# Optimization experiments

Measured on AMD Instinct MI355X. Metric: run time of the kernel, lower is better.

The kernel has to match this reference:

```python
import jax, jax.numpy as jnp
import numpy as np
from jax import lax

FEATURE_NUM = 16
FILTERS = 64
BATCH = 64
WINDOW = 5
T = 2048
SECTORS = 11
D = 256          # embedding dim / number of quantization buckets
DA = 64
VOCAB = 100000
L = T - 3 * WINDOW + 3  # 2036, length after conv->maxpool->conv (all valid, stride 1)
BN_EPS = 1e-5


def _conv1d(x, w):
    # x: [N, C, W], w: [O, I, K], valid padding, stride 1
    return lax.conv_general_dilated(x, w, (1,), 'VALID', dimension_numbers=('NCH', 'OIH', 'NCH'))


def setup_inputs() -> dict:
    key = jax.random.key(0)
    ks = jax.random.split(key, 9)
    x = jax.random.normal(ks[0], (BATCH, 2 * FEATURE_NUM, T), jnp.float32)
    conv1_w = jax.random.normal(ks[1], (FILTERS, 2 * FEATURE_NUM, WINDOW), jnp.float32) * 0.1
    conv1_b = jnp.zeros((FILTERS,), jnp.float32)
    bn_gamma = jnp.ones((FILTERS,), jnp.float32)
    bn_beta = jnp.zeros((FILTERS,), jnp.float32)
    conv2_w = jax.random.normal(ks[2], (1, FILTERS, WINDOW), jnp.float32) * 0.1
    conv2_b = jnp.zeros((1,), jnp.float32)
    emb = jax.random.normal(ks[3], (VOCAB, D), jnp.float32)
    W1 = jax.random.normal(ks[4], (DA, L), jnp.float32)
    W2 = jax.random.normal(ks[5], (DA, 1), jnp.float32)
    lin_w = jax.random.normal(ks[6], (SECTORS, D), jnp.float32) * 0.05
    lin_b = jnp.zeros((SECTORS,), jnp.float32)
    return {'x': x, 'conv1_w': conv1_w, 'conv1_b': conv1_b, 'bn_gamma': bn_gamma,
            'bn_beta': bn_beta, 'conv2_w': conv2_w, 'conv2_b': conv2_b, 'emb': emb,
            'W1': W1, 'W2': W2, 'lin_w': lin_w, 'lin_b': lin_b}


def reference(x, conv1_w, conv1_b, bn_gamma, bn_beta, conv2_w, conv2_b, emb, W1, W2, lin_w, lin_b):
    # conv1 (valid) -> maxpool(k=WINDOW, s=1) -> batchnorm (train-mode batch stats) -> conv2 -> relu
    h = _conv1d(x, conv1_w) + conv1_b[None, :, None]                     # [B, F, T-W+1]
    h = lax.reduce_window(h, -jnp.inf, lax.max, (1, 1, WINDOW), (1, 1, 1), 'VALID')
    mu = jnp.mean(h, axis=(0, 2), keepdims=True)
    var = jnp.mean((h - mu) ** 2, axis=(0, 2), keepdims=True)            # biased, as torch BN train
    h = (h - mu) * lax.rsqrt(var + BN_EPS) * bn_gamma[None, :, None] + bn_beta[None, :, None]
    h = jax.nn.relu(_conv1d(h, conv2_w) + conv2_b[None, :, None])        # [B, 1, L]
    c = jax.nn.sigmoid(h[:, 0, :])                                       # [B, L] in (0,1)
    # embedding_generate: first j with c <= (j+1)/D  <=>  j = ceil(c*D) - 1
    idx = jnp.clip(jnp.ceil(c * D).astype(jnp.int32) - 1, 0, D - 1)      # [B, L]
    e = emb[idx]                                                         # [B, L, D]
    # per-sample attention: A = W2^T tanh(W1 @ out), batched as einsums
    t = jnp.tanh(jnp.einsum('al,bld->bad', W1, e))                       # [B, DA, D]
    A = jnp.einsum('a,bad->bd', W2[:, 0], t)                             # [B, D]
    att = jax.nn.softmax(jnp.einsum('bld,bd->bl', e, A), axis=1)         # [B, L]
    scores = A @ lin_w.T + lin_b                                         # [B, SECTORS]
    return att, scores
```

## Files before the change

kernel.cpp:

```cpp
#include <hip/hip_runtime.h>
#include <hip/hip_bf16.h>
#include <math.h>

#define BATCH 64
#define CIN   32
#define TIN   2048
#define FILT  64
#define WIN   5
#define TP1   2044
#define TP2   2040
#define LOUT  2036
#define DEMB  256
#define DA    64
#define NSEC  11
#define NC    4
#define CS    509
#define TILE_T 252

__global__ __launch_bounds__(256) void k_conv1pool(
    const float* __restrict__ x, const float* __restrict__ w1,
    const float* __restrict__ b1, float* __restrict__ h2,
    float* __restrict__ bnps, float* __restrict__ bnpq) {
  __shared__ float xl[CIN * 264];
  const int b   = blockIdx.y;
  const int t0  = blockIdx.x * TILE_T;
  const int tid = threadIdx.x;

  for (int i = tid; i < CIN * 264; i += 256) {
    int c = i / 264, o = i - c * 264;
    int gt = t0 + o;
    float v = 0.f;
    if (o < 260 && gt < TIN) v = x[(b * CIN + c) * TIN + gt];
    xl[i] = v;
  }
  __syncthreads();

  const int tg  = tid & 63;
  const int tb  = tg * 4;
  const int wf0 = __builtin_amdgcn_readfirstlane(tid >> 6) * 16;
  const float* wb = w1 + wf0 * (CIN * WIN);

  float acc[16][4];
#pragma unroll
  for (int ff = 0; ff < 16; ++ff) {
    float bias = b1[wf0 + ff];
    acc[ff][0] = bias; acc[ff][1] = bias; acc[ff][2] = bias; acc[ff][3] = bias;
  }

  for (int c = 0; c < CIN; ++c) {
    float4 xa  = *(const float4*)&xl[c * 264 + tb];
    float4 xb4 = *(const float4*)&xl[c * 264 + tb + 4];
    float xw[8] = {xa.x, xa.y, xa.z, xa.w, xb4.x, xb4.y, xb4.z, xb4.w};
#pragma unroll
    for (int ff = 0; ff < 16; ++ff) {
      const float* wr = wb + ff * (CIN * WIN) + c * WIN;
#pragma unroll
      for (int k = 0; k < WIN; ++k) {
        float wv = wr[k];
        acc[ff][0] = fmaf(xw[k + 0], wv, acc[ff][0]);
        acc[ff][1] = fmaf(xw[k + 1], wv, acc[ff][1]);
        acc[ff][2] = fmaf(xw[k + 2], wv, acc[ff][2]);
        acc[ff][3] = fmaf(xw[k + 3], wv, acc[ff][3]);
      }
    }
  }

  const bool rowvalid = (tg < 63);
  const int blk = blockIdx.y * 9 + blockIdx.x;
#pragma unroll
  for (int ff = 0; ff < 16; ++ff) {
    float n0 = __shfl_down(acc[ff][0], 1);
    float n1 = __shfl_down(acc[ff][1], 1);
    float n2 = __shfl_down(acc[ff][2], 1);
    float n3 = __shfl_down(acc[ff][3], 1);
    float h[8] = {acc[ff][0], acc[ff][1], acc[ff][2], acc[ff][3], n0, n1, n2, n3};
    float o0 = fmaxf(fmaxf(fmaxf(h[0], h[1]), fmaxf(h[2], h[3])), h[4]);
    float o1 = fmaxf(fmaxf(fmaxf(h[1], h[2]), fmaxf(h[3], h[4])), h[5]);
    float o2 = fmaxf(fmaxf(fmaxf(h[2], h[3]), fmaxf(h[4], h[5])), h[6]);
    float o3 = fmaxf(fmaxf(fmaxf(h[3], h[4]), fmaxf(h[5], h[6])), h[7]);
    const int f = wf0 + ff;
    float s = 0.f, q = 0.f;
    const int t2b = t0 + tb;
    if (rowvalid && (t2b + 3 < TP2)) {
      *(float4*)&h2[(b * FILT + f) * TP2 + t2b] = make_float4(o0, o1, o2, o3);
      s = o0 + o1 + o2 + o3;
      q = o0 * o0 + o1 * o1 + o2 * o2 + o3 * o3;
    } else if (rowvalid) {
      float ov[4] = {o0, o1, o2, o3};
#pragma unroll
      for (int j = 0; j < 4; ++j) {
        int t2 = t2b + j;
        if (t2 < TP2) { h2[(b * FILT + f) * TP2 + t2] = ov[j]; s += ov[j]; q += ov[j] * ov[j]; }
      }
    }
#pragma unroll
    for (int off = 32; off > 0; off >>= 1) {
      s += __shfl_down(s, off);
      q += __shfl_down(q, off);
    }
    if (tg == 0) { bnps[blk * FILT + f] = s; bnpq[blk * FILT + f] = q; }
  }
}

__global__ void k_bnfin(const float* __restrict__ bnps, const float* __restrict__ bnpq,
                        const float* __restrict__ gamma, const float* __restrict__ beta,
                        const float* __restrict__ w2, const float* __restrict__ b2,
                        double* __restrict__ ws2, double* __restrict__ c0p) {
  const int f = threadIdx.x;
  double s = 0.0, q = 0.0;
  for (int blk = 0; blk < 576; ++blk) {
    s += (double)bnps[blk * FILT + f];
    q += (double)bnpq[blk * FILT + f];
  }
  const double N = (double)(BATCH * TP2);
  double mu  = s / N;
  double var = q / N - mu * mu;
  double sc  = (double)gamma[f] / sqrt(var + 1e-5);
  double sh  = (double)beta[f] - mu * sc;
  double wsum = 0.0;
#pragma unroll
  for (int k = 0; k < WIN; ++k) {
    double wv = (double)w2[f * WIN + k];
    ws2[f * WIN + k] = sc * wv;
    wsum += wv;
  }
  double part = sh * wsum;
#pragma unroll
  for (int off = 32; off > 0; off >>= 1) part += __shfl_down(part, off);
  if (f == 0) c0p[0] = part + (double)b2[0];
}

__global__ __launch_bounds__(256) void k_conv2(
    const float* __restrict__ h2, const double* __restrict__ ws2,
    const double* __restrict__ c0p, int* __restrict__ idxp, int* __restrict__ count) {
  __shared__ float hl[FILT * 260];
  __shared__ int hist[DEMB];
  const int b = blockIdx.y;
  const int t0 = blockIdx.x * 256;
  const int tid = threadIdx.x;
  for (int i = tid; i < FILT * 260; i += 256) {
    int f = i / 260, o = i - f * 260;
    int gt = t0 + o;
    hl[i] = (gt < TP2) ? h2[(b * FILT + f) * TP2 + gt] : 0.f;
  }
  hist[tid] = 0;
  __syncthreads();
  const int t = t0 + tid;
  if (t < LOUT) {
    double z = c0p[0];
    for (int f = 0; f < FILT; ++f) {
      const double* wr = ws2 + f * WIN;
      z = fma((double)hl[f * 260 + tid + 0], wr[0], z);
      z = fma((double)hl[f * 260 + tid + 1], wr[1], z);
      z = fma((double)hl[f * 260 + tid + 2], wr[2], z);
      z = fma((double)hl[f * 260 + tid + 3], wr[3], z);
      z = fma((double)hl[f * 260 + tid + 4], wr[4], z);
    }
    z = z > 0.0 ? z : 0.0;
    double c = 1.0 / (1.0 + exp(-z));
    int iv = (int)ceil(c * 256.0) - 1;
    iv = min(max(iv, 0), DEMB - 1);
    idxp[b * LOUT + t] = iv;
    atomicAdd(&hist[iv], 1);
  }
  __syncthreads();
  atomicAdd(&count[b * DEMB + tid], hist[tid]);
}

__global__ void k_t1(const float* __restrict__ W1, float* __restrict__ W1T) {
  int i = blockIdx.x * 256 + threadIdx.x;
  int l = i >> 6, a = i & 63;
  W1T[i] = W1[a * LOUT + l];
}
__global__ void k_t2(const float* __restrict__ emb, float* __restrict__ embT) {
  int i = blockIdx.x * 256 + threadIdx.x;
  int d = i >> 8, j = i & 255;
  embT[i] = emb[j * DEMB + d];
}

__global__ __launch_bounds__(256) void k_sbuild(
    const int* __restrict__ idxp, const float* __restrict__ w1t,
    float* __restrict__ Sg) {
  __shared__ float S[DA * 257];
  __shared__ int il[512];
  const int b = blockIdx.y, ch = blockIdx.x;
  const int tid = threadIdx.x;
  for (int i = tid; i < DA * 257; i += 256) S[i] = 0.f;
  const int l0 = ch * CS;
  for (int i = tid; i < CS; i += 256) il[i] = idxp[b * LOUT + l0 + i];
  __syncthreads();
  const int a = tid & 63, w = tid >> 6;
#pragma unroll 4
  for (int li = w; li < CS; li += 4) {
    int j = il[li];
    float v = w1t[(l0 + li) * DA + a];
    atomicAdd(&S[a * 257 + j], v);
  }
  __syncthreads();
  for (int i = tid; i < DA * DEMB; i += 256) {
    int aa = i >> 8, j = i & 255;
    Sg[((b * NC + ch) * DA + aa) * DEMB + j] = S[aa * 257 + j];
  }
}

__global__ __launch_bounds__(256) void k_gemmA(
    const float* __restrict__ Sg, const float* __restrict__ emb,
    const float* __restrict__ W2, float* __restrict__ Avec) {
  __shared__ float Al[16 * 64];
  __shared__ float Bl[16 * 64];
  __shared__ float red[16 * 64];
  const int b = blockIdx.x, c0 = blockIdx.y * 64;
  const int tid = threadIdx.x;
  const int tx = tid & 15, ty = tid >> 4;
  const int sa = tid >> 2, skq = (tid & 3) * 4;
  const int bk = tid >> 4, bseg = tid & 15;
  float acc[4][4] = {{0}};

  for (int kc = 0; kc < 16; ++kc) {
    const int kb = kc * 16;
    float4 v0 = *(const float4*)&Sg[((b * NC + 0) * DA + sa) * DEMB + kb + skq];
    float4 v1 = *(const float4*)&Sg[((b * NC + 1) * DA + sa) * DEMB + kb + skq];
    float4 v2 = *(const float4*)&Sg[((b * NC + 2) * DA + sa) * DEMB + kb + skq];
    float4 v3 = *(const float4*)&Sg[((b * NC + 3) * DA + sa) * DEMB + kb + skq];
    float4 sv = make_float4(v0.x + v1.x + v2.x + v3.x, v0.y + v1.y + v2.y + v3.y,
                            v0.z + v1.z + v2.z + v3.z, v0.w + v1.w + v2.w + v3.w);
    Al[(skq + 0) * 64 + sa] = sv.x;
    Al[(skq + 1) * 64 + sa] = sv.y;
    Al[(skq + 2) * 64 + sa] = sv.z;
    Al[(skq + 3) * 64 + sa] = sv.w;
    float4 e4 = *(const float4*)&emb[(kb + bk) * DEMB + c0 + bseg * 4];
    *(float4*)&Bl[bk * 64 + bseg * 4] = e4;
    __syncthreads();
#pragma unroll
    for (int k = 0; k < 16; ++k) {
      float4 av = *(const float4*)&Al[k * 64 + ty * 4];
      float4 bv = *(const float4*)&Bl[k * 64 + tx * 4];
      acc[0][0] = fmaf(av.x, bv.x, acc[0][0]); acc[0][1] = fmaf(av.x, bv.y, acc[0][1]);
      acc[0][2] = fmaf(av.x, bv.z, acc[0][2]); acc[0][3] = fmaf(av.x, bv.w, acc[0][3]);
      acc[1][0] = fmaf(av.y, bv.x, acc[1][0]); acc[1][1] = fmaf(av.y, bv.y, acc[1][1]);
      acc[1][2] = fmaf(av.y, bv.z, acc[1][2]); acc[1][3] = fmaf(av.y, bv.w, acc[1][3]);
      acc[2][0] = fmaf(av.z, bv.x, acc[2][0]); acc[2][1] = fmaf(av.z, bv.y, acc[2][1]);
      acc[2][2] = fmaf(av.z, bv.z, acc[2][2]); acc[2][3] = fmaf(av.z, bv.w, acc[2][3]);
      acc[3][0] = fmaf(av.w, bv.x, acc[3][0]); acc[3][1] = fmaf(av.w, bv.y, acc[3][1]);
      acc[3][2] = fmaf(av.w, bv.z, acc[3][2]); acc[3][3] = fmaf(av.w, bv.w, acc[3][3]);
    }
    __syncthreads();
  }
  float cs[4] = {0.f, 0.f, 0.f, 0.f};
#pragma unroll
  for (int r = 0; r < 4; ++r) {
    float wv = W2[ty * 4 + r];
#pragma unroll
    for (int j = 0; j < 4; ++j) cs[j] += tanhf(acc[r][j]) * wv;
  }
#pragma unroll
  for (int j = 0; j < 4; ++j) red[ty * 64 + tx * 4 + j] = cs[j];
  __syncthreads();
  if (tid < 64) {
    float s = 0.f;
#pragma unroll
    for (int q = 0; q < 16; ++q) s += red[q * 64 + tid];
    Avec[b * DEMB + c0 + tid] = s;
  }
}

__global__ __launch_bounds__(256) void k_att(
    const float* __restrict__ Avec, const float* __restrict__ embT,
    const int* __restrict__ count, const float* __restrict__ linw,
    const float* __restrict__ linb, float* __restrict__ p,
    float* __restrict__ scores) {
  __shared__ float Al[DEMB];
  __shared__ float scratch[4];
  const int b = blockIdx.x, j = threadIdx.x;
  Al[j] = Avec[b * DEMB + j];
  __syncthreads();
  float dot = 0.f;
  for (int d = 0; d < DEMB; ++d) dot = fmaf(embT[d * DEMB + j], Al[d], dot);
  const int cnt = count[b * DEMB + j];
  float v = (cnt > 0) ? dot : -3.4e38f;
#pragma unroll
  for (int off = 32; off > 0; off >>= 1) v = fmaxf(v, __shfl_down(v, off));
  if ((j & 63) == 0) scratch[j >> 6] = v;
  __syncthreads();
  const float m = fmaxf(fmaxf(scratch[0], scratch[1]), fmaxf(scratch[2], scratch[3]));
  __syncthreads();
  float e = (cnt > 0) ? expf(dot - m) : 0.f;
  float zs = e * (float)cnt;
#pragma unroll
  for (int off = 32; off > 0; off >>= 1) zs += __shfl_down(zs, off);
  if ((j & 63) == 0) scratch[j >> 6] = zs;
  __syncthreads();
  const float Z = scratch[0] + scratch[1] + scratch[2] + scratch[3];
  p[b * DEMB + j] = (cnt > 0) ? e / Z : 0.f;
  for (int s = 0; s < NSEC; ++s) {
    __syncthreads();
    float part = Al[j] * linw[s * DEMB + j];
#pragma unroll
    for (int off = 32; off > 0; off >>= 1) part += __shfl_down(part, off);
    if ((j & 63) == 0) scratch[j >> 6] = part;
    __syncthreads();
    if (j == 0)
      scores[b * NSEC + s] = scratch[0] + scratch[1] + scratch[2] + scratch[3] + linb[s];
  }
}

__global__ void k_gather(const int* __restrict__ idxp, const float* __restrict__ p,
                         float* __restrict__ att) {
  const int b = blockIdx.y;
  const int t = blockIdx.x * 256 + threadIdx.x;
  if (t < LOUT) att[b * LOUT + t] = p[b * DEMB + idxp[b * LOUT + t]];
}

extern "C" void kernel_launch(void* const* d_in, const int* in_sizes, int n_in,
                              void* d_out, int out_size, void* d_ws, size_t ws_size,
                              hipStream_t stream) {
  const float* x      = (const float*)d_in[0];
  const float* w1     = (const float*)d_in[1];
  const float* b1     = (const float*)d_in[2];
  const float* gamma  = (const float*)d_in[3];
  const float* beta   = (const float*)d_in[4];
  const float* w2     = (const float*)d_in[5];
  const float* b2     = (const float*)d_in[6];
  const float* emb    = (const float*)d_in[7];
  const float* W1     = (const float*)d_in[8];
  const float* W2     = (const float*)d_in[9];
  const float* linw   = (const float*)d_in[10];
  const float* linb   = (const float*)d_in[11];

  char* ws = (char*)d_ws;
  int*    count = (int*)   (ws + 0);
  double* ws2   = (double*)(ws + 65536);
  double* c0p   = (double*)(ws + 68096);
  float*  bnps  = (float*) (ws + 68608);
  float*  bnpq  = (float*) (ws + 216064);
  int*    idxp  = (int*)   (ws + 363520);
  float*  w1t   = (float*) (ws + 884736);
  float*  embT  = (float*) (ws + 1405952);
  float*  Avec  = (float*) (ws + 1668096);
  float*  p     = (float*) (ws + 1733632);
  float*  h2    = (float*) (ws + 1799168);
  float*  Sg    = (float*) (ws + 35222528);

  float* att_out    = (float*)d_out;
  float* scores_out = (float*)d_out + BATCH * LOUT;

  hipMemsetAsync(count, 0, 65536, stream);
  k_t1<<<dim3(509), 256, 0, stream>>>(W1, w1t);
  k_t2<<<dim3(256), 256, 0, stream>>>(emb, embT);
  k_conv1pool<<<dim3(9, 64), 256, 0, stream>>>(x, w1, b1, h2, bnps, bnpq);
  k_bnfin<<<dim3(1), 64, 0, stream>>>(bnps, bnpq, gamma, beta, w2, b2, ws2, c0p);
  k_conv2<<<dim3(8, 64), 256, 0, stream>>>(h2, ws2, c0p, idxp, count);
  k_sbuild<<<dim3(NC, 64), 256, 0, stream>>>(idxp, w1t, Sg);
  k_gemmA<<<dim3(64, 4), 256, 0, stream>>>(Sg, emb, W2, Avec);
  k_att<<<dim3(64), 256, 0, stream>>>(Avec, embT, count, linw, linb, p, scores_out);
  k_gather<<<dim3(8, 64), 256, 0, stream>>>(idxp, p, att_out);
}
```

Baseline: 359.1 us.

## Merge prep kernels, split conv1 over filter halves, fuse gather into attention

Replaces the memset and two transpose kernels with one prep kernel that zeroes counts, transposes W1 and emb through LDS tiles, and reorders conv1 weights channel-major. Conv1 gets a third grid dimension splitting the filters into two halves, which doubles block count and halves accumulator registers. BN finalize now uses 256 threads to parallelize the partial-sum reduction, and the att gather is folded into k_att using LDS probabilities. Together these cut launch count and aim to improve occupancy and memory coalescing, at the cost of each conv1 block reloading the x tile twice.

```diff
diff --git a/kernel.cpp b/kernel.cpp
--- a/kernel.cpp
+++ b/kernel.cpp
@@ -17,8 +17,44 @@
 #define CS    509
 #define TILE_T 252
 
+__global__ __launch_bounds__(256) void k_prep(
+    const float* __restrict__ W1, const float* __restrict__ emb,
+    const float* __restrict__ w1, float* __restrict__ w1t,
+    float* __restrict__ embT, float* __restrict__ w1r, int* __restrict__ count) {
+  __shared__ float tl[64 * 65];
+  int bk = blockIdx.x;
+  const int tid = threadIdx.x;
+  if (bk < 64) { count[bk * 256 + tid] = 0; return; }
+  bk -= 64;
+  if (bk < 32) {
+    const int l0 = bk * 64;
+    const int lc = tid & 63, rq = tid >> 6;
+    for (int a = rq; a < 64; a += 4)
+      tl[a * 65 + lc] = (l0 + lc < LOUT) ? W1[a * LOUT + l0 + lc] : 0.f;
+    __syncthreads();
+    for (int lp = rq; lp < 64; lp += 4)
+      if (l0 + lp < LOUT) w1t[(l0 + lp) * 64 + lc] = tl[lc * 65 + lp];
+    return;
+  }
+  bk -= 32;
+  if (bk < 16) {
+    const int j0 = (bk & 3) * 64, d0 = (bk >> 2) * 64;
+    const int c = tid & 63, rq = tid >> 6;
+    for (int j = rq; j < 64; j += 4) tl[j * 65 + c] = emb[(j0 + j) * DEMB + d0 + c];
+    __syncthreads();
+    for (int d = rq; d < 64; d += 4) embT[(d0 + d) * DEMB + j0 + c] = tl[c * 65 + d];
+    return;
+  }
+  bk -= 16;
+  {
+    int i = bk * 256 + tid;
+    int c = i / 320, r = i - c * 320, f = r / 5, k = r - f * 5;
+    w1r[i] = w1[f * (CIN * WIN) + c * WIN + k];
+  }
+}
+
 __global__ __launch_bounds__(256) void k_conv1pool(
-    const float* __restrict__ x, const float* __restrict__ w1,
+    const float* __restrict__ x, const float* __restrict__ w1r,
     const float* __restrict__ b1, float* __restrict__ h2,
     float* __restrict__ bnps, float* __restrict__ bnpq) {
   __shared__ float xl[CIN * 264];
@@ -37,12 +73,11 @@
 
   const int tg  = tid & 63;
   const int tb  = tg * 4;
-  const int wf0 = __builtin_amdgcn_readfirstlane(tid >> 6) * 16;
-  const float* wb = w1 + wf0 * (CIN * WIN);
-
-  float acc[16][4];
-#pragma unroll
-  for (int ff = 0; ff < 16; ++ff) {
+  const int wf0 = __builtin_amdgcn_readfirstlane((int)blockIdx.z * 32 + (tid >> 6) * 8);
+
+  float acc[8][4];
+#pragma unroll
+  for (int ff = 0; ff < 8; ++ff) {
     float bias = b1[wf0 + ff];
     acc[ff][0] = bias; acc[ff][1] = bias; acc[ff][2] = bias; acc[ff][3] = bias;
   }
@@ -51,12 +86,12 @@
     float4 xa  = *(const float4*)&xl[c * 264 + tb];
     float4 xb4 = *(const float4*)&xl[c * 264 + tb + 4];
     float xw[8] = {xa.x, xa.y, xa.z, xa.w, xb4.x, xb4.y, xb4.z, xb4.w};
-#pragma unroll
-    for (int ff = 0; ff < 16; ++ff) {
-      const float* wr = wb + ff * (CIN * WIN) + c * WIN;
+    const float* wr = w1r + c * 320 + wf0 * 5;
+#pragma unroll
+    for (int ff = 0; ff < 8; ++ff) {
 #pragma unroll
       for (int k = 0; k < WIN; ++k) {
-        float wv = wr[k];
+        float wv = wr[ff * 5 + k];
         acc[ff][0] = fmaf(xw[k + 0], wv, acc[ff][0]);
         acc[ff][1] = fmaf(xw[k + 1], wv, acc[ff][1]);
         acc[ff][2] = fmaf(xw[k + 2], wv, acc[ff][2]);
@@ -66,9 +101,9 @@
   }
 
   const bool rowvalid = (tg < 63);
-  const int blk = blockIdx.y * 9 + blockIdx.x;
-#pragma unroll
-  for (int ff = 0; ff < 16; ++ff) {
+  const int blk = b * 9 + blockIdx.x;
+#pragma unroll
+  for (int ff = 0; ff < 8; ++ff) {
     float n0 = __shfl_down(acc[ff][0], 1);
     float n1 = __shfl_down(acc[ff][1], 1);
     float n2 = __shfl_down(acc[ff][2], 1);
@@ -102,32 +137,41 @@
   }
 }
 
-__global__ void k_bnfin(const float* __restrict__ bnps, const float* __restrict__ bnpq,
-                        const float* __restrict__ gamma, const float* __restrict__ beta,
-                        const float* __restrict__ w2, const float* __restrict__ b2,
-                        double* __restrict__ ws2, double* __restrict__ c0p) {
-  const int f = threadIdx.x;
+__global__ __launch_bounds__(256) void k_bnfin(
+    const float* __restrict__ bnps, const float* __restrict__ bnpq,
+    const float* __restrict__ gamma, const float* __restrict__ beta,
+    const float* __restrict__ w2, const float* __restrict__ b2,
+    double* __restrict__ ws2, double* __restrict__ c0p) {
+  __shared__ double ls[4 * 64], lq[4 * 64];
+  const int tid = threadIdx.x;
+  const int f = tid & 63, g = tid >> 6;
   double s = 0.0, q = 0.0;
-  for (int blk = 0; blk < 576; ++blk) {
+  for (int blk = g; blk < 576; blk += 4) {
     s += (double)bnps[blk * FILT + f];
     q += (double)bnpq[blk * FILT + f];
   }
-  const double N = (double)(BATCH * TP2);
-  double mu  = s / N;
-  double var = q / N - mu * mu;
-  double sc  = (double)gamma[f] / sqrt(var + 1e-5);
-  double sh  = (double)beta[f] - mu * sc;
-  double wsum = 0.0;
-#pragma unroll
-  for (int k = 0; k < WIN; ++k) {
-    double wv = (double)w2[f * WIN + k];
-    ws2[f * WIN + k] = sc * wv;
-    wsum += wv;
-  }
-  double part = sh * wsum;
-#pragma unroll
-  for (int off = 32; off > 0; off >>= 1) part += __shfl_down(part, off);
-  if (f == 0) c0p[0] = part + (double)b2[0];
+  ls[g * 64 + f] = s; lq[g * 64 + f] = q;
+  __syncthreads();
+  if (tid < 64) {
+    s = ls[tid] + ls[64 + tid] + ls[128 + tid] + ls[192 + tid];
+    q = lq[tid] + lq[64 + tid] + lq[128 + tid] + lq[192 + tid];
+    const double N = (double)(BATCH * TP2);
+    double mu  = s / N;
+    double var = q / N - mu * mu;
+    double sc  = (double)gamma[tid] / sqrt(var + 1e-5);
+    double sh  = (double)beta[tid] - mu * sc;
+    double wsum = 0.0;
+#pragma unroll
+    for (int k = 0; k < WIN; ++k) {
+      double wv = (double)w2[tid * WIN + k];
+      ws2[tid * WIN + k] = sc * wv;
+      wsum += wv;
+    }
+    double part = sh * wsum;
+#pragma unroll
+    for (int off = 32; off > 0; off >>= 1) part += __shfl_down(part, off);
+    if (tid == 0) c0p[0] = part + (double)b2[0];
+  }
 }
 
 __global__ __launch_bounds__(256) void k_conv2(
@@ -165,17 +209,6 @@
   }
   __syncthreads();
   atomicAdd(&count[b * DEMB + tid], hist[tid]);
-}
-
-__global__ void k_t1(const float* __restrict__ W1, float* __restrict__ W1T) {
-  int i = blockIdx.x * 256 + threadIdx.x;
-  int l = i >> 6, a = i & 63;
-  W1T[i] = W1[a * LOUT + l];
-}
-__global__ void k_t2(const float* __restrict__ emb, float* __restrict__ embT) {
-  int i = blockIdx.x * 256 + threadIdx.x;
-  int d = i >> 8, j = i & 255;
-  embT[i] = emb[j * DEMB + d];
 }
 
 __global__ __launch_bounds__(256) void k_sbuild(
@@ -267,9 +300,10 @@
 __global__ __launch_bounds__(256) void k_att(
     const float* __restrict__ Avec, const float* __restrict__ embT,
     const int* __restrict__ count, const float* __restrict__ linw,
-    const float* __restrict__ linb, float* __restrict__ p,
-    float* __restrict__ scores) {
+    const float* __restrict__ linb, const int* __restrict__ idxp,
+    float* __restrict__ att, float* __restrict__ scores) {
   __shared__ float Al[DEMB];
+  __shared__ float pl[DEMB];
   __shared__ float scratch[4];
   const int b = blockIdx.x, j = threadIdx.x;
   Al[j] = Avec[b * DEMB + j];
@@ -291,7 +325,10 @@
   if ((j & 63) == 0) scratch[j >> 6] = zs;
   __syncthreads();
   const float Z = scratch[0] + scratch[1] + scratch[2] + scratch[3];
-  p[b * DEMB + j] = (cnt > 0) ? e / Z : 0.f;
+  pl[j] = (cnt > 0) ? e / Z : 0.f;
+  __syncthreads();
+  for (int l = j; l < LOUT; l += 256)
+    att[b * LOUT + l] = pl[idxp[b * LOUT + l]];
   for (int s = 0; s < NSEC; ++s) {
     __syncthreads();
     float part = Al[j] * linw[s * DEMB + j];
@@ -302,13 +339,6 @@
     if (j == 0)
       scores[b * NSEC + s] = scratch[0] + scratch[1] + scratch[2] + scratch[3] + linb[s];
   }
-}
-
-__global__ void k_gather(const int* __restrict__ idxp, const float* __restrict__ p,
-                         float* __restrict__ att) {
-  const int b = blockIdx.y;
-  const int t = blockIdx.x * 256 + threadIdx.x;
-  if (t < LOUT) att[b * LOUT + t] = p[b * DEMB + idxp[b * LOUT + t]];
 }
 
 extern "C" void kernel_launch(void* const* d_in, const int* in_sizes, int n_in,
@@ -337,21 +367,19 @@
   float*  w1t   = (float*) (ws + 884736);
   float*  embT  = (float*) (ws + 1405952);
   float*  Avec  = (float*) (ws + 1668096);
-  float*  p     = (float*) (ws + 1733632);
-  float*  h2    = (float*) (ws + 1799168);
-  float*  Sg    = (float*) (ws + 35222528);
+  float*  w1r   = (float*) (ws + 1733632);
+  float*  h2    = (float*) (ws + 1774592);
+  float*  Sg    = (float*) (ws + 35197952);
 
   float* att_out    = (float*)d_out;
   float* scores_out = (float*)d_out + BATCH * LOUT;
 
-  hipMemsetAsync(count, 0, 65536, stream);
-  k_t1<<<dim3(509), 256, 0, stream>>>(W1, w1t);
-  k_t2<<<dim3(256), 256, 0, stream>>>(emb, embT);
-  k_conv1pool<<<dim3(9, 64), 256, 0, stream>>>(x, w1, b1, h2, bnps, bnpq);
-  k_bnfin<<<dim3(1), 64, 0, stream>>>(bnps, bnpq, gamma, beta, w2, b2, ws2, c0p);
+  k_prep<<<dim3(152), 256, 0, stream>>>(W1, emb, w1, w1t, embT, w1r, count);
+  k_conv1pool<<<dim3(9, 64, 2), 256, 0, stream>>>(x, w1r, b1, h2, bnps, bnpq);
+  k_bnfin<<<dim3(1), 256, 0, stream>>>(bnps, bnpq, gamma, beta, w2, b2, ws2, c0p);
   k_conv2<<<dim3(8, 64), 256, 0, stream>>>(h2, ws2, c0p, idxp, count);
   k_sbuild<<<dim3(NC, 64), 256, 0, stream>>>(idxp, w1t, Sg);
   k_gemmA<<<dim3(64, 4), 256, 0, stream>>>(Sg, emb, W2, Avec);
-  k_att<<<dim3(64), 256, 0, stream>>>(Avec, embT, count, linw, linb, p, scores_out);
-  k_gather<<<dim3(8, 64), 256, 0, stream>>>(idxp, p, att_out);
-}
+  k_att<<<dim3(64), 256, 0, stream>>>(Avec, embT, count, linw, linb, idxp,
+                                      att_out, scores_out);
+}
```

Measured after the change: 377.0 us. 5.0% more time.
